# Performance work log

Hardware: AMD Instinct MI355X
Metric: run time of the kernel (lower is better)

Reference implementation:

```python
import jax, jax.numpy as jnp
import numpy as np

T, B, F, L = 512, 4096, 16, 4  # seq_len, batch, input_size, n_layers; hidden_size H = 1


def _lstm_layer(seq, W_ih, W_hh, b_ih, b_hh):
    """Single unidirectional LSTM layer, H=1.
    seq: [T, B, in]; W_ih: [4, in]; W_hh: [4, 1]; b_ih, b_hh: [4].
    Returns (hs [T,B,1], h_T [B,1], c_T [B,1]). Gate order i,f,g,o (PyTorch).
    """
    # Input contribution for all timesteps at once (the only sizeable GEMM).
    gx = jnp.einsum('tbi,gi->tbg', seq, W_ih) + b_ih + b_hh  # [T, B, 4]
    Bb = seq.shape[1]
    h0 = jnp.zeros((Bb, 1), seq.dtype)
    c0 = jnp.zeros((Bb, 1), seq.dtype)

    def step(carry, g):
        h, c = carry
        gates = g + h @ W_hh.T  # [B, 4]
        i = jax.nn.sigmoid(gates[:, 0:1])
        f = jax.nn.sigmoid(gates[:, 1:2])
        gg = jnp.tanh(gates[:, 2:3])
        o = jax.nn.sigmoid(gates[:, 3:4])
        c = f * c + i * gg
        h = o * jnp.tanh(c)
        return (h, c), h

    (hT, cT), hs = jax.lax.scan(step, (h0, c0), gx)
    return hs, hT, cT


def setup_inputs() -> dict:
    key = jax.random.key(0)
    ks = jax.random.split(key, 6)
    s = 0.5  # ~U(-1,1) stdev scale; 1/sqrt(H)=1 in torch init
    return {
        'x': jax.random.normal(ks[0], (T, B, F), jnp.float32),
        'W_ih0': jax.random.normal(ks[1], (4, F), jnp.float32) * s,
        'W_ih_rest': jax.random.normal(ks[2], (L - 1, 4, 1), jnp.float32) * s,
        'W_hh': jax.random.normal(ks[3], (L, 4, 1), jnp.float32) * s,
        'b_ih': jax.random.normal(ks[4], (L, 4), jnp.float32) * s,
        'b_hh': jax.random.normal(ks[5], (L, 4), jnp.float32) * s,
    }


def reference(x, W_ih0, W_ih_rest, W_hh, b_ih, b_hh):
    seq = x
    hns, cns = [], []
    for l in range(L):
        W_ih_l = W_ih0 if l == 0 else W_ih_rest[l - 1]
        seq, hT, cT = _lstm_layer(seq, W_ih_l, W_hh[l], b_ih[l], b_hh[l])
        hns.append(hT)
        cns.append(cT)
    output = seq                      # [T, B, 1] last-layer hidden sequence
    hn = jnp.stack(hns, axis=0)       # [L, B, 1]
    cn = jnp.stack(cns, axis=0)       # [L, B, 1]
    return output, hn, cn
```

## Files before the change

kernel.cpp:

```cpp
#include <hip/hip_runtime.h>

#define T_DIM 512
#define B_DIM 4096
#define L_DIM 4
#define LOG2E 1.44269504088896f
#define TWOLOG2E 2.88539008177793f
#define HALF_LN2 0.346573590279973f

template <int CTRL>
__device__ __forceinline__ float dpp_mov(float v) {
  int r = __builtin_amdgcn_update_dpp(0, __builtin_bit_cast(int, v), CTRL, 0xf, 0xf, true);
  return __builtin_bit_cast(float, r);
}
template <int CTRL>
__device__ __forceinline__ float qp_add(float v) { return v + dpp_mov<CTRL>(v); }

__global__ __launch_bounds__(256, 1) void lstm_fused(
    const float* __restrict__ x,
    const float* __restrict__ Wih0,
    const float* __restrict__ Wrest,
    const float* __restrict__ Whh,
    const float* __restrict__ bih, const float* __restrict__ bhh,
    float* __restrict__ out) {
  const int tid = threadIdx.x;
  const int lane = tid & 63;
  const int wid = tid >> 6;
  const int g = lane & 3;
  const int l = (lane >> 2) & 3;
  const int c = (lane >> 4) & 3;
  const int chain = blockIdx.x * 16 + wid * 4 + c;
  const bool l0 = (l == 0);

  auto sg = [](int i) { return (i == 2) ? 2.0f * LOG2E : -LOG2E; };

  const float whh  = sg(g) * Whh[l * 4 + g];
  const float wih  = l0 ? 0.f : sg(g) * Wrest[(l - 1) * 4 + g];
  const float base = l0 ? 0.f : sg(g) * (bih[l * 4 + g] + bhh[l * 4 + g]);

  float wq0, wq1, wq2, wq3;
  {
    const float s = sg(g);
    wq0 = s * Wih0[g * 16 + 4 * l + ((g + 0) & 3)];
    wq1 = s * Wih0[g * 16 + 4 * l + ((g + 1) & 3)];
    wq2 = s * Wih0[g * 16 + 4 * l + ((g + 2) & 3)];
    wq3 = s * Wih0[g * 16 + 4 * l + ((g + 3) & 3)];
  }
  const float dinit = l0 ? sg(g) * (bih[g] + bhh[g]) : 0.f;
  const float vm = (g == 2) ? -2.f * TWOLOG2E : 1.f;
  const float va = (g == 2) ? TWOLOG2E : 0.f;

  const float* __restrict__ xp = x + (size_t)chain * 16 + (size_t)(4 * l + g);
  float* __restrict__ po = out + chain;

  float h = 0.f, cse = 0.f;
  float A[8], B[8];

#define LOAD8(R, t0)                                                        \
  do {                                                                      \
    R[0] = xp[(size_t)((t0) + 0) * 65536];                                  \
    R[1] = xp[(size_t)((t0) + 1) * 65536];                                  \
    R[2] = xp[(size_t)((t0) + 2) * 65536];                                  \
    R[3] = xp[(size_t)((t0) + 3) * 65536];                                  \
    R[4] = xp[(size_t)((t0) + 4) * 65536];                                  \
    R[5] = xp[(size_t)((t0) + 5) * 65536];                                  \
    R[6] = xp[(size_t)((t0) + 6) * 65536];                                  \
    R[7] = xp[(size_t)((t0) + 7) * 65536];                                  \
  } while (0)

  auto dotD = [&](float xv) -> float {
    float x1 = dpp_mov<0x39>(xv);
    float x2 = dpp_mov<0x4E>(xv);
    float x3 = dpp_mov<0x93>(xv);
    float p = fmaf(xv, wq0, dinit);
    p = fmaf(x1, wq1, p);
    p = fmaf(x2, wq2, p);
    p = fmaf(x3, wq3, p);
    p = qp_add<0x124>(p);
    p = qp_add<0x128>(p);
    return p;
  };

  auto cellv = [&](int k, float D, bool guard) {
    float hin = dpp_mov<0x114>(h);
    float pb = l0 ? D : base;
    float gate = fmaf(whh, h, fmaf(wih, hin, pb));

    float r = __builtin_amdgcn_rcpf(1.0f + __builtin_amdgcn_exp2f(gate));
    float v = fmaf(vm, r, va);

    float i_  = dpp_mov<0x00>(v);
    float f_  = dpp_mov<0x55>(v);
    float tgs = dpp_mov<0xAA>(v);
    float o_  = dpp_mov<0xFF>(v);
    float cne = fmaf(f_, cse, i_ * tgs);
    float tcn = fmaf(-2.0f,
        __builtin_amdgcn_rcpf(1.0f + __builtin_amdgcn_exp2f(cne)), 1.0f);
    float hm = o_ * tcn;

    if (guard) {
      const bool valid = (unsigned)(k - l) < (unsigned)T_DIM;
      cse = valid ? cne : cse;
      h   = valid ? hm : h;
    } else {
      cse = cne; h = hm;
    }
    const int t = k - 3;
    if (l == 3 && g == 0 && (unsigned)t < (unsigned)T_DIM)
      po[(size_t)t * B_DIM] = hm;
  };

#define CELLS8(R, k0, guard)                                                \
  do {                                                                      \
    float D0_ = dotD(R[0]), D1_ = dotD(R[1]), D2_ = dotD(R[2]),             \
          D3_ = dotD(R[3]), D4_ = dotD(R[4]), D5_ = dotD(R[5]),             \
          D6_ = dotD(R[6]), D7_ = dotD(R[7]);                               \
    cellv((k0) + 0, D0_, guard);                                            \
    cellv((k0) + 1, D1_, guard);                                            \
    cellv((k0) + 2, D2_, guard);                                            \
    cellv((k0) + 3, D3_, guard);                                            \
    cellv((k0) + 4, D4_, guard);                                            \
    cellv((k0) + 5, D5_, guard);                                            \
    cellv((k0) + 6, D6_, guard);                                            \
    cellv((k0) + 7, D7_, guard);                                            \
  } while (0)

  LOAD8(A, 0);
  LOAD8(B, 8);
  CELLS8(A, 0, true);
#pragma unroll 1
  for (int n = 1; n < 63; n += 2) {
    LOAD8(A, 8 * (n + 1));
    CELLS8(B, 8 * n, false);
    LOAD8(B, 8 * (n + 2));
    CELLS8(A, 8 * (n + 1), false);
  }
  CELLS8(B, 504, false);
  CELLS8(B, 512, true);

  if (g == 0) {
    po[(size_t)T_DIM * B_DIM + (size_t)l * B_DIM] = h;
    po[(size_t)T_DIM * B_DIM + (size_t)L_DIM * B_DIM + (size_t)l * B_DIM] =
        cse * HALF_LN2;
  }
#undef LOAD8
#undef CELLS8
}

extern "C" void kernel_launch(void* const* d_in, const int* in_sizes, int n_in,
                              void* d_out, int out_size, void* d_ws, size_t ws_size,
                              hipStream_t stream) {
  const float* x     = (const float*)d_in[0];
  const float* Wih0  = (const float*)d_in[1];
  const float* Wrest = (const float*)d_in[2];
  const float* Whh   = (const float*)d_in[3];
  const float* bih   = (const float*)d_in[4];
  const float* bhh   = (const float*)d_in[5];
  float* out = (float*)d_out;
  lstm_fused<<<B_DIM / 16, 256, 0, stream>>>(x, Wih0, Wrest, Whh, bih, bhh, out);
}
```

Before: 218.3 us.

## Stage x through LDS with async global_load_lds and batch output stores

Replaces the per-lane strided global loads of x with direct global-to-LDS DMA (global_load_lds), double-buffered per wave, then reads each lane's four inputs as a float4 from shared memory. This removes the three DPP rotations per timestep used to share inputs across lanes. Output stores are deferred and flushed after an explicit vmcnt(0) wait, so stores and loads no longer interleave inside the recurrence. The tradeoff is extra LDS traffic, a full vmcnt wait each block of 8 steps that also waits on pending stores, and more register pressure from holding buffered hidden values.

```diff
diff --git a/kernel.cpp b/kernel.cpp
--- a/kernel.cpp
+++ b/kernel.cpp
@@ -7,6 +7,8 @@
 #define TWOLOG2E 2.88539008177793f
 #define HALF_LN2 0.346573590279973f
 
+typedef float f4 __attribute__((ext_vector_type(4)));
+
 template <int CTRL>
 __device__ __forceinline__ float dpp_mov(float v) {
   int r = __builtin_amdgcn_update_dpp(0, __builtin_bit_cast(int, v), CTRL, 0xf, 0xf, true);
@@ -14,6 +16,14 @@
 }
 template <int CTRL>
 __device__ __forceinline__ float qp_add(float v) { return v + dpp_mov<CTRL>(v); }
+
+__device__ __forceinline__ void dma4(const float* gsrc, float* ldst) {
+  __builtin_amdgcn_global_load_lds(
+      (const __attribute__((address_space(1))) void*)gsrc,
+      (__attribute__((address_space(3))) void*)ldst, 4, 0, 0);
+}
+
+#define WAITV0 asm volatile("s_waitcnt vmcnt(0)" ::: "memory")
 
 __global__ __launch_bounds__(256, 1) void lstm_fused(
     const float* __restrict__ x,
@@ -31,56 +41,69 @@
   const int chain = blockIdx.x * 16 + wid * 4 + c;
   const bool l0 = (l == 0);
 
+  __shared__ float sh[4096];
+
   auto sg = [](int i) { return (i == 2) ? 2.0f * LOG2E : -LOG2E; };
 
   const float whh  = sg(g) * Whh[l * 4 + g];
   const float wih  = l0 ? 0.f : sg(g) * Wrest[(l - 1) * 4 + g];
   const float base = l0 ? 0.f : sg(g) * (bih[l * 4 + g] + bhh[l * 4 + g]);
-
-  float wq0, wq1, wq2, wq3;
+  f4 wx;
   {
     const float s = sg(g);
-    wq0 = s * Wih0[g * 16 + 4 * l + ((g + 0) & 3)];
-    wq1 = s * Wih0[g * 16 + 4 * l + ((g + 1) & 3)];
-    wq2 = s * Wih0[g * 16 + 4 * l + ((g + 2) & 3)];
-    wq3 = s * Wih0[g * 16 + 4 * l + ((g + 3) & 3)];
+    wx.x = s * Wih0[g * 16 + 4 * l + 0];
+    wx.y = s * Wih0[g * 16 + 4 * l + 1];
+    wx.z = s * Wih0[g * 16 + 4 * l + 2];
+    wx.w = s * Wih0[g * 16 + 4 * l + 3];
   }
   const float dinit = l0 ? sg(g) * (bih[g] + bhh[g]) : 0.f;
   const float vm = (g == 2) ? -2.f * TWOLOG2E : 1.f;
   const float va = (g == 2) ? TWOLOG2E : 0.f;
 
-  const float* __restrict__ xp = x + (size_t)chain * 16 + (size_t)(4 * l + g);
+  const float* __restrict__ xg = x + (size_t)blockIdx.x * 256 + wid * 64 + lane;
   float* __restrict__ po = out + chain;
 
+  const int shw = wid * 1024;
+  const int rdb = shw + c * 16 + 4 * l;
+
   float h = 0.f, cse = 0.f;
-  float A[8], B[8];
-
-#define LOAD8(R, t0)                                                        \
-  do {                                                                      \
-    R[0] = xp[(size_t)((t0) + 0) * 65536];                                  \
-    R[1] = xp[(size_t)((t0) + 1) * 65536];                                  \
-    R[2] = xp[(size_t)((t0) + 2) * 65536];                                  \
-    R[3] = xp[(size_t)((t0) + 3) * 65536];                                  \
-    R[4] = xp[(size_t)((t0) + 4) * 65536];                                  \
-    R[5] = xp[(size_t)((t0) + 5) * 65536];                                  \
-    R[6] = xp[(size_t)((t0) + 6) * 65536];                                  \
-    R[7] = xp[(size_t)((t0) + 7) * 65536];                                  \
-  } while (0)
-
-  auto dotD = [&](float xv) -> float {
-    float x1 = dpp_mov<0x39>(xv);
-    float x2 = dpp_mov<0x4E>(xv);
-    float x3 = dpp_mov<0x93>(xv);
-    float p = fmaf(xv, wq0, dinit);
-    p = fmaf(x1, wq1, p);
-    p = fmaf(x2, wq2, p);
-    p = fmaf(x3, wq3, p);
+  float hs0, hs1, hs2, hs3, hs4, hs5, hs6, hs7;
+  f4 X0, X1, X2, X3, X4, X5, X6, X7;
+
+#define DMA8(B, t0)                                                         \
+  do {                                                                      \
+    const float* _g = xg + (size_t)(t0) * 65536;                            \
+    float* _d = &sh[shw + (B) * 512];                                       \
+    dma4(_g + 0 * 65536, _d + 0 * 64);                                      \
+    dma4(_g + 1 * 65536, _d + 1 * 64);                                      \
+    dma4(_g + 2 * 65536, _d + 2 * 64);                                      \
+    dma4(_g + 3 * 65536, _d + 3 * 64);                                      \
+    dma4(_g + 4 * 65536, _d + 4 * 64);                                      \
+    dma4(_g + 5 * 65536, _d + 5 * 64);                                      \
+    dma4(_g + 6 * 65536, _d + 6 * 64);                                      \
+    dma4(_g + 7 * 65536, _d + 7 * 64);                                      \
+  } while (0)
+
+#define READ8(B)                                                            \
+  do {                                                                      \
+    X0 = *(const f4*)&sh[rdb + (B) * 512 + 0 * 64];                         \
+    X1 = *(const f4*)&sh[rdb + (B) * 512 + 1 * 64];                         \
+    X2 = *(const f4*)&sh[rdb + (B) * 512 + 2 * 64];                         \
+    X3 = *(const f4*)&sh[rdb + (B) * 512 + 3 * 64];                         \
+    X4 = *(const f4*)&sh[rdb + (B) * 512 + 4 * 64];                         \
+    X5 = *(const f4*)&sh[rdb + (B) * 512 + 5 * 64];                         \
+    X6 = *(const f4*)&sh[rdb + (B) * 512 + 6 * 64];                         \
+    X7 = *(const f4*)&sh[rdb + (B) * 512 + 7 * 64];                         \
+  } while (0)
+
+  auto dotD = [&](f4 xv) -> float {
+    float p = fmaf(xv.x, wx.x, fmaf(xv.y, wx.y, fmaf(xv.z, wx.z, fmaf(xv.w, wx.w, dinit))));
     p = qp_add<0x124>(p);
     p = qp_add<0x128>(p);
     return p;
   };
 
-  auto cellv = [&](int k, float D, bool guard) {
+  auto cellv = [&](int k, float D, bool guard) -> float {
     float hin = dpp_mov<0x114>(h);
     float pb = l0 ? D : base;
     float gate = fmaf(whh, h, fmaf(wih, hin, pb));
@@ -104,46 +127,66 @@
     } else {
       cse = cne; h = hm;
     }
-    const int t = k - 3;
-    if (l == 3 && g == 0 && (unsigned)t < (unsigned)T_DIM)
-      po[(size_t)t * B_DIM] = hm;
+    return hm;
   };
 
-#define CELLS8(R, k0, guard)                                                \
-  do {                                                                      \
-    float D0_ = dotD(R[0]), D1_ = dotD(R[1]), D2_ = dotD(R[2]),             \
-          D3_ = dotD(R[3]), D4_ = dotD(R[4]), D5_ = dotD(R[5]),             \
-          D6_ = dotD(R[6]), D7_ = dotD(R[7]);                               \
-    cellv((k0) + 0, D0_, guard);                                            \
-    cellv((k0) + 1, D1_, guard);                                            \
-    cellv((k0) + 2, D2_, guard);                                            \
-    cellv((k0) + 3, D3_, guard);                                            \
-    cellv((k0) + 4, D4_, guard);                                            \
-    cellv((k0) + 5, D5_, guard);                                            \
-    cellv((k0) + 6, D6_, guard);                                            \
-    cellv((k0) + 7, D7_, guard);                                            \
-  } while (0)
-
-  LOAD8(A, 0);
-  LOAD8(B, 8);
-  CELLS8(A, 0, true);
+#define CELLS8(k0, guard)                                                   \
+  do {                                                                      \
+    float D0_ = dotD(X0), D1_ = dotD(X1), D2_ = dotD(X2), D3_ = dotD(X3),   \
+          D4_ = dotD(X4), D5_ = dotD(X5), D6_ = dotD(X6), D7_ = dotD(X7);   \
+    hs0 = cellv((k0) + 0, D0_, guard);                                      \
+    hs1 = cellv((k0) + 1, D1_, guard);                                      \
+    hs2 = cellv((k0) + 2, D2_, guard);                                      \
+    hs3 = cellv((k0) + 3, D3_, guard);                                      \
+    hs4 = cellv((k0) + 4, D4_, guard);                                      \
+    hs5 = cellv((k0) + 5, D5_, guard);                                      \
+    hs6 = cellv((k0) + 6, D6_, guard);                                      \
+    hs7 = cellv((k0) + 7, D7_, guard);                                      \
+  } while (0)
+
+#define FLUSH(k0, jlo, jhi)                                                 \
+  do {                                                                      \
+    if (l == 3 && g == 0) {                                                 \
+      if (0 >= (jlo) && 0 <= (jhi)) po[(size_t)((k0) + 0 - 3) * B_DIM] = hs0; \
+      if (1 >= (jlo) && 1 <= (jhi)) po[(size_t)((k0) + 1 - 3) * B_DIM] = hs1; \
+      if (2 >= (jlo) && 2 <= (jhi)) po[(size_t)((k0) + 2 - 3) * B_DIM] = hs2; \
+      if (3 >= (jlo) && 3 <= (jhi)) po[(size_t)((k0) + 3 - 3) * B_DIM] = hs3; \
+      if (4 >= (jlo) && 4 <= (jhi)) po[(size_t)((k0) + 4 - 3) * B_DIM] = hs4; \
+      if (5 >= (jlo) && 5 <= (jhi)) po[(size_t)((k0) + 5 - 3) * B_DIM] = hs5; \
+      if (6 >= (jlo) && 6 <= (jhi)) po[(size_t)((k0) + 6 - 3) * B_DIM] = hs6; \
+      if (7 >= (jlo) && 7 <= (jhi)) po[(size_t)((k0) + 7 - 3) * B_DIM] = hs7; \
+    }                                                                       \
+  } while (0)
+
+  DMA8(0, 0);
+  WAITV0;
+  READ8(0);
+  DMA8(1, 8);
+  CELLS8(0, true);
+  WAITV0; FLUSH(0, 3, 7);  READ8(1); DMA8(0, 16); CELLS8(8, false);
+  WAITV0; FLUSH(8, 0, 7);  READ8(0); DMA8(1, 24); CELLS8(16, false);
 #pragma unroll 1
-  for (int n = 1; n < 63; n += 2) {
-    LOAD8(A, 8 * (n + 1));
-    CELLS8(B, 8 * n, false);
-    LOAD8(B, 8 * (n + 2));
-    CELLS8(A, 8 * (n + 1), false);
+  for (int n = 3; n < 63; n += 2) {
+    WAITV0; FLUSH(8 * (n - 1), 0, 7); READ8(1); DMA8(0, 8 * (n + 1));
+    CELLS8(8 * n, false);
+    WAITV0; FLUSH(8 * n, 0, 7);       READ8(0); DMA8(1, 8 * (n + 2));
+    CELLS8(8 * (n + 1), false);
   }
-  CELLS8(B, 504, false);
-  CELLS8(B, 512, true);
+  WAITV0; FLUSH(8 * 62, 0, 7); READ8(1);
+  CELLS8(504, false);
+  FLUSH(504, 0, 7);
+  CELLS8(512, true);
+  FLUSH(512, 0, 2);
 
   if (g == 0) {
     po[(size_t)T_DIM * B_DIM + (size_t)l * B_DIM] = h;
     po[(size_t)T_DIM * B_DIM + (size_t)L_DIM * B_DIM + (size_t)l * B_DIM] =
         cse * HALF_LN2;
   }
-#undef LOAD8
+#undef DMA8
+#undef READ8
 #undef CELLS8
+#undef FLUSH
 }
 
 extern "C" void kernel_launch(void* const* d_in, const int* in_sizes, int n_in,
```

New measurement: 232.7 us. 1.07x slower.

## Interleave two independent chain groups per wavefront for ILP, halve block size

Applied to the files above, without the earlier changes.

Each wavefront now handles two sets of four batch chains (P and Q, offset by four chains), interleaving their serial LSTM cell updates so the dependent DPP and transcendental latencies of one hide behind the other. The block shrinks from 256 to 128 threads with the same grid, so there are half as many wavefronts, each doing twice the work. Scheduling barriers are placed after the prefetch loads to keep them grouped ahead of compute. The cost is more register pressure and fewer resident waves available to hide memory latency.

```diff
diff --git a/kernel.cpp b/kernel.cpp
--- a/kernel.cpp
+++ b/kernel.cpp
@@ -15,7 +15,9 @@
 template <int CTRL>
 __device__ __forceinline__ float qp_add(float v) { return v + dpp_mov<CTRL>(v); }
 
-__global__ __launch_bounds__(256, 1) void lstm_fused(
+#define SCHED_FENCE __builtin_amdgcn_sched_barrier(0)
+
+__global__ __launch_bounds__(128, 1) void lstm_fused(
     const float* __restrict__ x,
     const float* __restrict__ Wih0,
     const float* __restrict__ Wrest,
@@ -28,7 +30,7 @@
   const int g = lane & 3;
   const int l = (lane >> 2) & 3;
   const int c = (lane >> 4) & 3;
-  const int chain = blockIdx.x * 16 + wid * 4 + c;
+  const int chainP = blockIdx.x * 16 + wid * 8 + c;
   const bool l0 = (l == 0);
 
   auto sg = [](int i) { return (i == 2) ? 2.0f * LOG2E : -LOG2E; };
@@ -49,22 +51,24 @@
   const float vm = (g == 2) ? -2.f * TWOLOG2E : 1.f;
   const float va = (g == 2) ? TWOLOG2E : 0.f;
 
-  const float* __restrict__ xp = x + (size_t)chain * 16 + (size_t)(4 * l + g);
-  float* __restrict__ po = out + chain;
+  const float* __restrict__ xp = x + (size_t)chainP * 16 + (size_t)(4 * l + g);
+  float* __restrict__ poP = out + chainP;
+  float* __restrict__ poQ = poP + 4;
 
-  float h = 0.f, cse = 0.f;
-  float A[8], B[8];
+  float hP = 0.f, cseP = 0.f;
+  float hQ = 0.f, cseQ = 0.f;
+  float AP[8], AQ[8], BP[8], BQ[8];
 
-#define LOAD8(R, t0)                                                        \
+#define LOAD8(R, t0, off)                                                   \
   do {                                                                      \
-    R[0] = xp[(size_t)((t0) + 0) * 65536];                                  \
-    R[1] = xp[(size_t)((t0) + 1) * 65536];                                  \
-    R[2] = xp[(size_t)((t0) + 2) * 65536];                                  \
-    R[3] = xp[(size_t)((t0) + 3) * 65536];                                  \
-    R[4] = xp[(size_t)((t0) + 4) * 65536];                                  \
-    R[5] = xp[(size_t)((t0) + 5) * 65536];                                  \
-    R[6] = xp[(size_t)((t0) + 6) * 65536];                                  \
-    R[7] = xp[(size_t)((t0) + 7) * 65536];                                  \
+    R[0] = xp[(size_t)((t0) + 0) * 65536 + (off)];                          \
+    R[1] = xp[(size_t)((t0) + 1) * 65536 + (off)];                          \
+    R[2] = xp[(size_t)((t0) + 2) * 65536 + (off)];                          \
+    R[3] = xp[(size_t)((t0) + 3) * 65536 + (off)];                          \
+    R[4] = xp[(size_t)((t0) + 4) * 65536 + (off)];                          \
+    R[5] = xp[(size_t)((t0) + 5) * 65536 + (off)];                          \
+    R[6] = xp[(size_t)((t0) + 6) * 65536 + (off)];                          \
+    R[7] = xp[(size_t)((t0) + 7) * 65536 + (off)];                          \
   } while (0)
 
   auto dotD = [&](float xv) -> float {
@@ -80,10 +84,11 @@
     return p;
   };
 
-  auto cellv = [&](int k, float D, bool guard) {
-    float hin = dpp_mov<0x114>(h);
+  auto cellv = [&](int k, float D, float& hS, float& cseS, float* __restrict__ poS,
+                   bool guard) {
+    float hin = dpp_mov<0x114>(hS);
     float pb = l0 ? D : base;
-    float gate = fmaf(whh, h, fmaf(wih, hin, pb));
+    float gate = fmaf(whh, hS, fmaf(wih, hin, pb));
 
     float r = __builtin_amdgcn_rcpf(1.0f + __builtin_amdgcn_exp2f(gate));
     float v = fmaf(vm, r, va);
@@ -92,55 +97,73 @@
     float f_  = dpp_mov<0x55>(v);
     float tgs = dpp_mov<0xAA>(v);
     float o_  = dpp_mov<0xFF>(v);
-    float cne = fmaf(f_, cse, i_ * tgs);
+    float cne = fmaf(f_, cseS, i_ * tgs);
     float tcn = fmaf(-2.0f,
         __builtin_amdgcn_rcpf(1.0f + __builtin_amdgcn_exp2f(cne)), 1.0f);
     float hm = o_ * tcn;
 
     if (guard) {
       const bool valid = (unsigned)(k - l) < (unsigned)T_DIM;
-      cse = valid ? cne : cse;
-      h   = valid ? hm : h;
+      cseS = valid ? cne : cseS;
+      hS   = valid ? hm : hS;
     } else {
-      cse = cne; h = hm;
+      cseS = cne; hS = hm;
     }
     const int t = k - 3;
     if (l == 3 && g == 0 && (unsigned)t < (unsigned)T_DIM)
-      po[(size_t)t * B_DIM] = hm;
+      poS[(size_t)t * B_DIM] = hm;
   };
 
-#define CELLS8(R, k0, guard)                                                \
+#define CELLS8(RP, RQ, k0, guard)                                           \
   do {                                                                      \
-    float D0_ = dotD(R[0]), D1_ = dotD(R[1]), D2_ = dotD(R[2]),             \
-          D3_ = dotD(R[3]), D4_ = dotD(R[4]), D5_ = dotD(R[5]),             \
-          D6_ = dotD(R[6]), D7_ = dotD(R[7]);                               \
-    cellv((k0) + 0, D0_, guard);                                            \
-    cellv((k0) + 1, D1_, guard);                                            \
-    cellv((k0) + 2, D2_, guard);                                            \
-    cellv((k0) + 3, D3_, guard);                                            \
-    cellv((k0) + 4, D4_, guard);                                            \
-    cellv((k0) + 5, D5_, guard);                                            \
-    cellv((k0) + 6, D6_, guard);                                            \
-    cellv((k0) + 7, D7_, guard);                                            \
+    float DP0 = dotD(RP[0]), DP1 = dotD(RP[1]), DP2 = dotD(RP[2]),          \
+          DP3 = dotD(RP[3]), DP4 = dotD(RP[4]), DP5 = dotD(RP[5]),          \
+          DP6 = dotD(RP[6]), DP7 = dotD(RP[7]);                             \
+    float DQ0 = dotD(RQ[0]), DQ1 = dotD(RQ[1]), DQ2 = dotD(RQ[2]),          \
+          DQ3 = dotD(RQ[3]), DQ4 = dotD(RQ[4]), DQ5 = dotD(RQ[5]),          \
+          DQ6 = dotD(RQ[6]), DQ7 = dotD(RQ[7]);                             \
+    cellv((k0) + 0, DP0, hP, cseP, poP, guard);                             \
+    cellv((k0) + 0, DQ0, hQ, cseQ, poQ, guard);                             \
+    cellv((k0) + 1, DP1, hP, cseP, poP, guard);                             \
+    cellv((k0) + 1, DQ1, hQ, cseQ, poQ, guard);                             \
+    cellv((k0) + 2, DP2, hP, cseP, poP, guard);                             \
+    cellv((k0) + 2, DQ2, hQ, cseQ, poQ, guard);                             \
+    cellv((k0) + 3, DP3, hP, cseP, poP, guard);                             \
+    cellv((k0) + 3, DQ3, hQ, cseQ, poQ, guard);                             \
+    cellv((k0) + 4, DP4, hP, cseP, poP, guard);                             \
+    cellv((k0) + 4, DQ4, hQ, cseQ, poQ, guard);                             \
+    cellv((k0) + 5, DP5, hP, cseP, poP, guard);                             \
+    cellv((k0) + 5, DQ5, hQ, cseQ, poQ, guard);                             \
+    cellv((k0) + 6, DP6, hP, cseP, poP, guard);                             \
+    cellv((k0) + 6, DQ6, hQ, cseQ, poQ, guard);                             \
+    cellv((k0) + 7, DP7, hP, cseP, poP, guard);                             \
+    cellv((k0) + 7, DQ7, hQ, cseQ, poQ, guard);                             \
   } while (0)
 
-  LOAD8(A, 0);
-  LOAD8(B, 8);
-  CELLS8(A, 0, true);
+  LOAD8(AP, 0, 0); LOAD8(AQ, 0, 64);
+  SCHED_FENCE;
+  LOAD8(BP, 8, 0); LOAD8(BQ, 8, 64);
+  SCHED_FENCE;
+  CELLS8(AP, AQ, 0, true);
 #pragma unroll 1
   for (int n = 1; n < 63; n += 2) {
-    LOAD8(A, 8 * (n + 1));
-    CELLS8(B, 8 * n, false);
-    LOAD8(B, 8 * (n + 2));
-    CELLS8(A, 8 * (n + 1), false);
+    LOAD8(AP, 8 * (n + 1), 0); LOAD8(AQ, 8 * (n + 1), 64);
+    SCHED_FENCE;
+    CELLS8(BP, BQ, 8 * n, false);
+    LOAD8(BP, 8 * (n + 2), 0); LOAD8(BQ, 8 * (n + 2), 64);
+    SCHED_FENCE;
+    CELLS8(AP, AQ, 8 * (n + 1), false);
   }
-  CELLS8(B, 504, false);
-  CELLS8(B, 512, true);
+  CELLS8(BP, BQ, 504, false);
+  CELLS8(BP, BQ, 512, true);
 
   if (g == 0) {
-    po[(size_t)T_DIM * B_DIM + (size_t)l * B_DIM] = h;
-    po[(size_t)T_DIM * B_DIM + (size_t)L_DIM * B_DIM + (size_t)l * B_DIM] =
-        cse * HALF_LN2;
+    poP[(size_t)T_DIM * B_DIM + (size_t)l * B_DIM] = hP;
+    poP[(size_t)T_DIM * B_DIM + (size_t)L_DIM * B_DIM + (size_t)l * B_DIM] =
+        cseP * HALF_LN2;
+    poQ[(size_t)T_DIM * B_DIM + (size_t)l * B_DIM] = hQ;
+    poQ[(size_t)T_DIM * B_DIM + (size_t)L_DIM * B_DIM + (size_t)l * B_DIM] =
+        cseQ * HALF_LN2;
   }
 #undef LOAD8
 #undef CELLS8
@@ -156,5 +179,5 @@
   const float* bih   = (const float*)d_in[4];
   const float* bhh   = (const float*)d_in[5];
   float* out = (float*)d_out;
-  lstm_fused<<<B_DIM / 16, 256, 0, stream>>>(x, Wih0, Wrest, Whh, bih, bhh, out);
+  lstm_fused<<<B_DIM / 16, 128, 0, stream>>>(x, Wih0, Wrest, Whh, bih, bhh, out);
 }
```

After: 255.9 us. 17.2% more time.
